# Performance work log

Measured on AMD Instinct MI355X. Metric: run time of the kernel, lower is better.

## Reference

```python
import jax, jax.numpy as jnp
import numpy as np
from jax import lax

H = 32  # hidden size (hardcoded in the torch module)

def setup_inputs() -> dict:
    key = jax.random.key(0)
    ks = jax.random.split(key, 7)
    B, T, I = 2048, 512, 64
    s = 1.0 / np.sqrt(H)  # torch nn.LSTM default init scale
    return {
        "x": jax.random.normal(ks[0], (B, T, I), dtype=jnp.float32),
        "W_ih": jax.random.uniform(ks[1], (4 * H, I), jnp.float32, -s, s),
        "W_hh": jax.random.uniform(ks[2], (4 * H, H), jnp.float32, -s, s),
        "b_ih": jax.random.uniform(ks[3], (4 * H,), jnp.float32, -s, s),
        "b_hh": jax.random.uniform(ks[4], (4 * H,), jnp.float32, -s, s),
        "W_fc": jax.random.uniform(ks[5], (1, H), jnp.float32, -s, s),
        "b_fc": jax.random.uniform(ks[6], (1,), jnp.float32, -s, s),
    }

def _lstm_last_h(x, W_ih, W_hh, b_ih, b_hh):
    B = x.shape[0]
    # Precompute input projections for all timesteps: [B, T, 4H] -> [T, B, 4H]
    xg = jnp.einsum('bti,gi->btg', x, W_ih) + (b_ih + b_hh)
    xg = jnp.transpose(xg, (1, 0, 2))

    def step(carry, xt):
        h, c = carry
        g = xt + h @ W_hh.T  # [B, 4H]
        i = jax.nn.sigmoid(g[:, 0 * H:1 * H])
        f = jax.nn.sigmoid(g[:, 1 * H:2 * H])
        gg = jnp.tanh(g[:, 2 * H:3 * H])
        o = jax.nn.sigmoid(g[:, 3 * H:4 * H])
        c = f * c + i * gg
        h = o * jnp.tanh(c)
        return (h, c), None

    init = (jnp.zeros((B, H), x.dtype), jnp.zeros((B, H), x.dtype))
    (h, _), _ = lax.scan(step, init, xg)
    return h  # [B, H], last timestep hidden state

def reference(x, W_ih, W_hh, b_ih, b_hh, W_fc, b_fc):
    # Dropout is identity in eval mode; only the last timestep feeds fc.
    h = _lstm_last_h(x, W_ih, W_hh, b_ih, b_hh)
    return h @ W_fc.T + b_fc  # [B, 1]
```

## Files before the change

kernel.cpp:

```cpp
#include <hip/hip_runtime.h>

typedef __attribute__((ext_vector_type(8))) short short8;
typedef __attribute__((ext_vector_type(4))) float f32x4;

#define LOG2E 1.44269504088896340736f

__device__ __forceinline__ unsigned short f2bf(float f) {
    union { float f; unsigned u; } a; a.f = f;
    unsigned r = a.u + 0x7fffu + ((a.u >> 16) & 1u);
    return (unsigned short)(r >> 16);
}
__device__ __forceinline__ unsigned pk2(float x, float y) {
    return (unsigned)f2bf(x) | ((unsigned)f2bf(y) << 16);
}
__device__ __forceinline__ float sigm(float x) {
    return __builtin_amdgcn_rcpf(1.0f + __builtin_amdgcn_exp2f(-LOG2E * x));
}

__global__ __launch_bounds__(256, 1) void lstm_fused(
    const float* __restrict__ x,
    const float* __restrict__ Wih,
    const float* __restrict__ Whh,
    const float* __restrict__ bih,
    const float* __restrict__ bhh,
    const float* __restrict__ Wfc,
    const float* __restrict__ bfc,
    float* __restrict__ out)
{
    __shared__ unsigned short Wlds[128 * 80];
    __shared__ float xg_sh[4 * 2 * 16 * 132];
    __shared__ alignas(64) unsigned short hbuf[4 * 64];

    const int tid  = threadIdx.x;
    const int lane = tid & 63;
    const int wv   = tid >> 6;
    const int b0   = blockIdx.x * 8 + wv * 2;
    const int m    = lane & 15;
    const int quad = lane >> 4;
    const int cc   = lane & 31;
    const int rb   = lane >> 5;

    {
        const float4* w4 = (const float4*)Wih;
        unsigned* wl = (unsigned*)Wlds;
        #pragma unroll
        for (int i = 0; i < 8; i++) {
            int fi = tid * 8 + i;
            int g  = fi >> 4;
            int k  = (fi & 15) << 2;
            float4 v = w4[fi];
            wl[g * 40 + (k >> 1) + 0] = pk2(v.x, v.y);
            wl[g * 40 + (k >> 1) + 1] = pk2(v.z, v.w);
        }
    }

    short8 Bh[8];
    #pragma unroll
    for (int t = 0; t < 8; t++) {
        const float4* wr = (const float4*)(Whh + (size_t)(16 * t + m) * 32 + quad * 8);
        float4 va = wr[0], vb = wr[1];
        union { short8 v; unsigned u[4]; } B;
        B.u[0] = pk2(va.x, va.y); B.u[1] = pk2(va.z, va.w);
        B.u[2] = pk2(vb.x, vb.y); B.u[3] = pk2(vb.z, vb.w);
        Bh[t] = B.v;
    }

    float biasv[8];
    #pragma unroll
    for (int n = 0; n < 8; n++) biasv[n] = bih[16 * n + m] + bhh[16 * n + m];

    const bool b4 = (lane & 16) != 0;

    __syncthreads();

    const float* xrow0 = x + ((size_t)b0 * 512 + m) * 64;
    const float* xrow1 = xrow0 + 512 * 64;
    float* xgw = xg_sh + wv * 4224;
    unsigned short* hw = hbuf + wv * 64;

    hw[lane] = 0;
    float c = 0.0f, h = 0.0f;
    const f32x4 z4 = {0.f, 0.f, 0.f, 0.f};

    float4 p0, p1, p2, p3, q0, q1, q2, q3;
    {
        const float4* r0 = (const float4*)xrow0;
        const float4* r1 = (const float4*)xrow1;
        p0 = r0[quad * 2];     p1 = r0[quad * 2 + 1];
        p2 = r0[8 + quad * 2]; p3 = r0[8 + quad * 2 + 1];
        q0 = r1[quad * 2];     q1 = r1[quad * 2 + 1];
        q2 = r1[8 + quad * 2]; q3 = r1[8 + quad * 2 + 1];
    }

    for (int ch = 0; ch < 32; ++ch) {
        union { short8 v; unsigned u[4]; } A0, A1, C0, C1;
        A0.u[0] = pk2(p0.x, p0.y); A0.u[1] = pk2(p0.z, p0.w);
        A0.u[2] = pk2(p1.x, p1.y); A0.u[3] = pk2(p1.z, p1.w);
        A1.u[0] = pk2(p2.x, p2.y); A1.u[1] = pk2(p2.z, p2.w);
        A1.u[2] = pk2(p3.x, p3.y); A1.u[3] = pk2(p3.z, p3.w);
        C0.u[0] = pk2(q0.x, q0.y); C0.u[1] = pk2(q0.z, q0.w);
        C0.u[2] = pk2(q1.x, q1.y); C0.u[3] = pk2(q1.z, q1.w);
        C1.u[0] = pk2(q2.x, q2.y); C1.u[1] = pk2(q2.z, q2.w);
        C1.u[2] = pk2(q3.x, q3.y); C1.u[3] = pk2(q3.z, q3.w);

        {
            const int chn = (ch < 31) ? ch + 1 : 31;
            const float4* n0 = (const float4*)(xrow0 + (size_t)chn * 1024);
            const float4* n1 = (const float4*)(xrow1 + (size_t)chn * 1024);
            p0 = n0[quad * 2];     p1 = n0[quad * 2 + 1];
            p2 = n0[8 + quad * 2]; p3 = n0[8 + quad * 2 + 1];
            q0 = n1[quad * 2];     q1 = n1[quad * 2 + 1];
            q2 = n1[8 + quad * 2]; q3 = n1[8 + quad * 2 + 1];
        }

        #pragma unroll
        for (int n = 0; n < 8; n++) {
            const short8 B0 = *(const short8*)&Wlds[(16 * n + m) * 80 + quad * 8];
            const short8 B1 = *(const short8*)&Wlds[(16 * n + m) * 80 + 32 + quad * 8];
            f32x4 ar0 = {0.f, 0.f, 0.f, 0.f};
            ar0 = __builtin_amdgcn_mfma_f32_16x16x32_bf16(A0.v, B0, ar0, 0, 0, 0);
            ar0 = __builtin_amdgcn_mfma_f32_16x16x32_bf16(A1.v, B1, ar0, 0, 0, 0);
            f32x4 ar1 = {0.f, 0.f, 0.f, 0.f};
            ar1 = __builtin_amdgcn_mfma_f32_16x16x32_bf16(C0.v, B0, ar1, 0, 0, 0);
            ar1 = __builtin_amdgcn_mfma_f32_16x16x32_bf16(C1.v, B1, ar1, 0, 0, 0);
            const int pos = ((n & 1) << 6) + 4 * m + (n >> 1);
            #pragma unroll
            for (int r = 0; r < 4; r++) {
                xgw[(quad * 4 + r) * 132 + pos]        = ar0[r] + biasv[n];
                xgw[2112 + (quad * 4 + r) * 132 + pos] = ar1[r] + biasv[n];
            }
        }

        #pragma unroll
        for (int tt = 0; tt < 16; ++tt) {
            const short8 abf = *(const short8*)&hw[((m >> 3) << 5) + quad * 8];
            const f32x4 a0 = __builtin_amdgcn_mfma_f32_16x16x32_bf16(abf, Bh[0], z4, 0, 0, 0);
            const f32x4 a1 = __builtin_amdgcn_mfma_f32_16x16x32_bf16(abf, Bh[1], z4, 0, 0, 0);
            const f32x4 a2 = __builtin_amdgcn_mfma_f32_16x16x32_bf16(abf, Bh[2], z4, 0, 0, 0);
            const f32x4 a3 = __builtin_amdgcn_mfma_f32_16x16x32_bf16(abf, Bh[3], z4, 0, 0, 0);
            const f32x4 a4 = __builtin_amdgcn_mfma_f32_16x16x32_bf16(abf, Bh[4], z4, 0, 0, 0);
            const f32x4 a5 = __builtin_amdgcn_mfma_f32_16x16x32_bf16(abf, Bh[5], z4, 0, 0, 0);
            const f32x4 a6 = __builtin_amdgcn_mfma_f32_16x16x32_bf16(abf, Bh[6], z4, 0, 0, 0);
            const f32x4 a7 = __builtin_amdgcn_mfma_f32_16x16x32_bf16(abf, Bh[7], z4, 0, 0, 0);
            const float hi = b4 ? a1[0] : a0[0];
            const float hf = b4 ? a3[0] : a2[0];
            const float hg = b4 ? a5[0] : a4[0];
            const float ho = b4 ? a7[0] : a6[0];

            const f32x4 xg4 = *(const f32x4*)&xgw[rb * 2112 + tt * 132 + 4 * cc];
            const float gi = xg4[0] + hi;
            const float gf = xg4[1] + hf;
            const float gg = xg4[2] + hg;
            const float go = xg4[3] + ho;

            const float iv = sigm(gi);
            const float fv = sigm(gf);
            const float gv = fmaf(2.0f, sigm(2.0f * gg), -1.0f);
            const float ov = sigm(go);
            c = fmaf(fv, c, iv * gv);
            const float th = fmaf(2.0f, sigm(2.0f * c), -1.0f);
            h = ov * th;
            hw[lane] = f2bf(h);
        }
    }

    float p = h * Wfc[cc];
    #pragma unroll
    for (int msk = 16; msk >= 1; msk >>= 1) p += __shfl_xor(p, msk);
    if ((lane & 31) == 0) out[b0 + rb] = p + bfc[0];
}

extern "C" void kernel_launch(void* const* d_in, const int* in_sizes, int n_in,
                              void* d_out, int out_size, void* d_ws, size_t ws_size,
                              hipStream_t stream) {
    const float* x   = (const float*)d_in[0];
    const float* Wih = (const float*)d_in[1];
    const float* Whh = (const float*)d_in[2];
    const float* bih = (const float*)d_in[3];
    const float* bhh = (const float*)d_in[4];
    const float* Wfc = (const float*)d_in[5];
    const float* bfc = (const float*)d_in[6];
    float* out = (float*)d_out;
    lstm_fused<<<dim3(256), dim3(256), 0, stream>>>(x, Wih, Whh, bih, bhh, Wfc, bfc, out);
}
```

Before: 419.7 us.

## Map one batch row per wave and run two blocks per CU

Measured after the change: 431.4 us. 1.03x slower.

```diff
diff --git a/kernel.cpp b/kernel.cpp
--- a/kernel.cpp
+++ b/kernel.cpp
@@ -17,7 +17,7 @@
     return __builtin_amdgcn_rcpf(1.0f + __builtin_amdgcn_exp2f(-LOG2E * x));
 }
 
-__global__ __launch_bounds__(256, 1) void lstm_fused(
+__global__ __launch_bounds__(256, 2) void lstm_fused(
     const float* __restrict__ x,
     const float* __restrict__ Wih,
     const float* __restrict__ Whh,
@@ -28,17 +28,16 @@
     float* __restrict__ out)
 {
     __shared__ unsigned short Wlds[128 * 80];
-    __shared__ float xg_sh[4 * 2 * 16 * 132];
+    __shared__ float xg_sh[4 * 16 * 132];
     __shared__ alignas(64) unsigned short hbuf[4 * 64];
 
     const int tid  = threadIdx.x;
     const int lane = tid & 63;
     const int wv   = tid >> 6;
-    const int b0   = blockIdx.x * 8 + wv * 2;
+    const int b0   = blockIdx.x * 4 + wv;
     const int m    = lane & 15;
     const int quad = lane >> 4;
     const int cc   = lane & 31;
-    const int rb   = lane >> 5;
 
     {
         const float4* w4 = (const float4*)Wih;
@@ -73,44 +72,33 @@
 
     __syncthreads();
 
-    const float* xrow0 = x + ((size_t)b0 * 512 + m) * 64;
-    const float* xrow1 = xrow0 + 512 * 64;
-    float* xgw = xg_sh + wv * 4224;
+    const float* xrow = x + ((size_t)b0 * 512 + m) * 64;
+    float* xgw = xg_sh + wv * 2112;
     unsigned short* hw = hbuf + wv * 64;
 
     hw[lane] = 0;
     float c = 0.0f, h = 0.0f;
     const f32x4 z4 = {0.f, 0.f, 0.f, 0.f};
 
-    float4 p0, p1, p2, p3, q0, q1, q2, q3;
+    float4 p0, p1, p2, p3;
     {
-        const float4* r0 = (const float4*)xrow0;
-        const float4* r1 = (const float4*)xrow1;
+        const float4* r0 = (const float4*)xrow;
         p0 = r0[quad * 2];     p1 = r0[quad * 2 + 1];
         p2 = r0[8 + quad * 2]; p3 = r0[8 + quad * 2 + 1];
-        q0 = r1[quad * 2];     q1 = r1[quad * 2 + 1];
-        q2 = r1[8 + quad * 2]; q3 = r1[8 + quad * 2 + 1];
     }
 
     for (int ch = 0; ch < 32; ++ch) {
-        union { short8 v; unsigned u[4]; } A0, A1, C0, C1;
+        union { short8 v; unsigned u[4]; } A0, A1;
         A0.u[0] = pk2(p0.x, p0.y); A0.u[1] = pk2(p0.z, p0.w);
         A0.u[2] = pk2(p1.x, p1.y); A0.u[3] = pk2(p1.z, p1.w);
         A1.u[0] = pk2(p2.x, p2.y); A1.u[1] = pk2(p2.z, p2.w);
         A1.u[2] = pk2(p3.x, p3.y); A1.u[3] = pk2(p3.z, p3.w);
-        C0.u[0] = pk2(q0.x, q0.y); C0.u[1] = pk2(q0.z, q0.w);
-        C0.u[2] = pk2(q1.x, q1.y); C0.u[3] = pk2(q1.z, q1.w);
-        C1.u[0] = pk2(q2.x, q2.y); C1.u[1] = pk2(q2.z, q2.w);
-        C1.u[2] = pk2(q3.x, q3.y); C1.u[3] = pk2(q3.z, q3.w);
 
         {
             const int chn = (ch < 31) ? ch + 1 : 31;
-            const float4* n0 = (const float4*)(xrow0 + (size_t)chn * 1024);
-            const float4* n1 = (const float4*)(xrow1 + (size_t)chn * 1024);
+            const float4* n0 = (const float4*)(xrow + (size_t)chn * 1024);
             p0 = n0[quad * 2];     p1 = n0[quad * 2 + 1];
             p2 = n0[8 + quad * 2]; p3 = n0[8 + quad * 2 + 1];
-            q0 = n1[quad * 2];     q1 = n1[quad * 2 + 1];
-            q2 = n1[8 + quad * 2]; q3 = n1[8 + quad * 2 + 1];
         }
 
         #pragma unroll
@@ -120,20 +108,16 @@
             f32x4 ar0 = {0.f, 0.f, 0.f, 0.f};
             ar0 = __builtin_amdgcn_mfma_f32_16x16x32_bf16(A0.v, B0, ar0, 0, 0, 0);
             ar0 = __builtin_amdgcn_mfma_f32_16x16x32_bf16(A1.v, B1, ar0, 0, 0, 0);
-            f32x4 ar1 = {0.f, 0.f, 0.f, 0.f};
-            ar1 = __builtin_amdgcn_mfma_f32_16x16x32_bf16(C0.v, B0, ar1, 0, 0, 0);
-            ar1 = __builtin_amdgcn_mfma_f32_16x16x32_bf16(C1.v, B1, ar1, 0, 0, 0);
             const int pos = ((n & 1) << 6) + 4 * m + (n >> 1);
             #pragma unroll
             for (int r = 0; r < 4; r++) {
-                xgw[(quad * 4 + r) * 132 + pos]        = ar0[r] + biasv[n];
-                xgw[2112 + (quad * 4 + r) * 132 + pos] = ar1[r] + biasv[n];
+                xgw[(quad * 4 + r) * 132 + pos] = ar0[r] + biasv[n];
             }
         }
 
         #pragma unroll
         for (int tt = 0; tt < 16; ++tt) {
-            const short8 abf = *(const short8*)&hw[((m >> 3) << 5) + quad * 8];
+            const short8 abf = *(const short8*)&hw[quad * 8];
             const f32x4 a0 = __builtin_amdgcn_mfma_f32_16x16x32_bf16(abf, Bh[0], z4, 0, 0, 0);
             const f32x4 a1 = __builtin_amdgcn_mfma_f32_16x16x32_bf16(abf, Bh[1], z4, 0, 0, 0);
             const f32x4 a2 = __builtin_amdgcn_mfma_f32_16x16x32_bf16(abf, Bh[2], z4, 0, 0, 0);
@@ -147,7 +131,7 @@
             const float hg = b4 ? a5[0] : a4[0];
             const float ho = b4 ? a7[0] : a6[0];
 
-            const f32x4 xg4 = *(const f32x4*)&xgw[rb * 2112 + tt * 132 + 4 * cc];
+            const f32x4 xg4 = *(const f32x4*)&xgw[tt * 132 + 4 * cc];
             const float gi = xg4[0] + hi;
             const float gf = xg4[1] + hf;
             const float gg = xg4[2] + hg;
@@ -167,7 +151,7 @@
     float p = h * Wfc[cc];
     #pragma unroll
     for (int msk = 16; msk >= 1; msk >>= 1) p += __shfl_xor(p, msk);
-    if ((lane & 31) == 0) out[b0 + rb] = p + bfc[0];
+    if (lane == 0) out[b0] = p + bfc[0];
 }
 
 extern "C" void kernel_launch(void* const* d_in, const int* in_sizes, int n_in,
@@ -181,5 +165,5 @@
     const float* Wfc = (const float*)d_in[5];
     const float* bfc = (const float*)d_in[6];
     float* out = (float*)d_out;
-    lstm_fused<<<dim3(256), dim3(256), 0, stream>>>(x, Wih, Whh, bih, bhh, Wfc, bfc, out);
+    lstm_fused<<<dim3(512), dim3(256), 0, stream>>>(x, Wih, Whh, bih, bhh, Wfc, bfc, out);
 }
```

## Keep LSTM hidden state in registers via transposed MFMA and lane shuffles

Applied to the files above, without the earlier changes.

Result: slower. 504.8 us (+20.3%).

```diff
diff --git a/kernel.cpp b/kernel.cpp
--- a/kernel.cpp
+++ b/kernel.cpp
@@ -5,13 +5,10 @@
 
 #define LOG2E 1.44269504088896340736f
 
-__device__ __forceinline__ unsigned short f2bf(float f) {
-    union { float f; unsigned u; } a; a.f = f;
-    unsigned r = a.u + 0x7fffu + ((a.u >> 16) & 1u);
-    return (unsigned short)(r >> 16);
-}
-__device__ __forceinline__ unsigned pk2(float x, float y) {
-    return (unsigned)f2bf(x) | ((unsigned)f2bf(y) << 16);
+__device__ __forceinline__ unsigned pkcvt(float lo, float hi) {
+    unsigned r;
+    asm("v_cvt_pk_bf16_f32 %0, %1, %2" : "=v"(r) : "v"(lo), "v"(hi));
+    return r;
 }
 __device__ __forceinline__ float sigm(float x) {
     return __builtin_amdgcn_rcpf(1.0f + __builtin_amdgcn_exp2f(-LOG2E * x));
@@ -28,17 +25,16 @@
     float* __restrict__ out)
 {
     __shared__ unsigned short Wlds[128 * 80];
-    __shared__ float xg_sh[4 * 2 * 16 * 132];
-    __shared__ alignas(64) unsigned short hbuf[4 * 64];
+    __shared__ float xg_sh[4 * 4768];
 
     const int tid  = threadIdx.x;
     const int lane = tid & 63;
     const int wv   = tid >> 6;
     const int b0   = blockIdx.x * 8 + wv * 2;
     const int m    = lane & 15;
-    const int quad = lane >> 4;
-    const int cc   = lane & 31;
-    const int rb   = lane >> 5;
+    const int q    = lane >> 4;
+    const int g    = m & 3;
+    const int rm   = (m >> 3) & 1;
 
     {
         const float4* w4 = (const float4*)Wih;
@@ -46,128 +42,161 @@
         #pragma unroll
         for (int i = 0; i < 8; i++) {
             int fi = tid * 8 + i;
-            int g  = fi >> 4;
+            int gg = fi >> 4;
             int k  = (fi & 15) << 2;
             float4 v = w4[fi];
-            wl[g * 40 + (k >> 1) + 0] = pk2(v.x, v.y);
-            wl[g * 40 + (k >> 1) + 1] = pk2(v.z, v.w);
-        }
-    }
-
-    short8 Bh[8];
+            wl[gg * 40 + (k >> 1) + 0] = pkcvt(v.x, v.y);
+            wl[gg * 40 + (k >> 1) + 1] = pkcvt(v.z, v.w);
+        }
+    }
+
+    short8 Wr[8];
     #pragma unroll
     for (int t = 0; t < 8; t++) {
-        const float4* wr = (const float4*)(Whh + (size_t)(16 * t + m) * 32 + quad * 8);
+        const int gr = (t >> 1) * 32 + 8 * (m >> 2) + (t & 1) * 4 + (m & 3);
+        const float4* wr = (const float4*)(Whh + (size_t)gr * 32 + q * 8);
         float4 va = wr[0], vb = wr[1];
         union { short8 v; unsigned u[4]; } B;
-        B.u[0] = pk2(va.x, va.y); B.u[1] = pk2(va.z, va.w);
-        B.u[2] = pk2(vb.x, vb.y); B.u[3] = pk2(vb.z, vb.w);
-        Bh[t] = B.v;
+        B.u[0] = pkcvt(va.x, va.y); B.u[1] = pkcvt(va.z, va.w);
+        B.u[2] = pkcvt(vb.x, vb.y); B.u[3] = pkcvt(vb.z, vb.w);
+        Wr[t] = B.v;
     }
 
     float biasv[8];
     #pragma unroll
     for (int n = 0; n < 8; n++) biasv[n] = bih[16 * n + m] + bhh[16 * n + m];
 
-    const bool b4 = (lane & 16) != 0;
-
     __syncthreads();
 
     const float* xrow0 = x + ((size_t)b0 * 512 + m) * 64;
     const float* xrow1 = xrow0 + 512 * 64;
-    float* xgw = xg_sh + wv * 4224;
-    unsigned short* hw = hbuf + wv * 64;
-
-    hw[lane] = 0;
-    float c = 0.0f, h = 0.0f;
+    float* xgw = xg_sh + wv * 4768;
+
+    float c0 = 0.0f, c1 = 0.0f, h0 = 0.0f, h1 = 0.0f;
     const f32x4 z4 = {0.f, 0.f, 0.f, 0.f};
 
     float4 p0, p1, p2, p3, q0, q1, q2, q3;
     {
         const float4* r0 = (const float4*)xrow0;
         const float4* r1 = (const float4*)xrow1;
-        p0 = r0[quad * 2];     p1 = r0[quad * 2 + 1];
-        p2 = r0[8 + quad * 2]; p3 = r0[8 + quad * 2 + 1];
-        q0 = r1[quad * 2];     q1 = r1[quad * 2 + 1];
-        q2 = r1[8 + quad * 2]; q3 = r1[8 + quad * 2 + 1];
-    }
+        p0 = r0[q * 2];     p1 = r0[q * 2 + 1];
+        p2 = r0[8 + q * 2]; p3 = r0[8 + q * 2 + 1];
+        q0 = r1[q * 2];     q1 = r1[q * 2 + 1];
+        q2 = r1[8 + q * 2]; q3 = r1[8 + q * 2 + 1];
+    }
+
+    const float* xb = xgw + rm * 2384 + q * 36 + g * 8;
+    const bool tsel = (g & 2) != 0;
+    const bool jsel = (g & 1) != 0;
 
     for (int ch = 0; ch < 32; ++ch) {
         union { short8 v; unsigned u[4]; } A0, A1, C0, C1;
-        A0.u[0] = pk2(p0.x, p0.y); A0.u[1] = pk2(p0.z, p0.w);
-        A0.u[2] = pk2(p1.x, p1.y); A0.u[3] = pk2(p1.z, p1.w);
-        A1.u[0] = pk2(p2.x, p2.y); A1.u[1] = pk2(p2.z, p2.w);
-        A1.u[2] = pk2(p3.x, p3.y); A1.u[3] = pk2(p3.z, p3.w);
-        C0.u[0] = pk2(q0.x, q0.y); C0.u[1] = pk2(q0.z, q0.w);
-        C0.u[2] = pk2(q1.x, q1.y); C0.u[3] = pk2(q1.z, q1.w);
-        C1.u[0] = pk2(q2.x, q2.y); C1.u[1] = pk2(q2.z, q2.w);
-        C1.u[2] = pk2(q3.x, q3.y); C1.u[3] = pk2(q3.z, q3.w);
+        A0.u[0] = pkcvt(p0.x, p0.y); A0.u[1] = pkcvt(p0.z, p0.w);
+        A0.u[2] = pkcvt(p1.x, p1.y); A0.u[3] = pkcvt(p1.z, p1.w);
+        A1.u[0] = pkcvt(p2.x, p2.y); A1.u[1] = pkcvt(p2.z, p2.w);
+        A1.u[2] = pkcvt(p3.x, p3.y); A1.u[3] = pkcvt(p3.z, p3.w);
+        C0.u[0] = pkcvt(q0.x, q0.y); C0.u[1] = pkcvt(q0.z, q0.w);
+        C0.u[2] = pkcvt(q1.x, q1.y); C0.u[3] = pkcvt(q1.z, q1.w);
+        C1.u[0] = pkcvt(q2.x, q2.y); C1.u[1] = pkcvt(q2.z, q2.w);
+        C1.u[2] = pkcvt(q3.x, q3.y); C1.u[3] = pkcvt(q3.z, q3.w);
 
         {
             const int chn = (ch < 31) ? ch + 1 : 31;
             const float4* n0 = (const float4*)(xrow0 + (size_t)chn * 1024);
             const float4* n1 = (const float4*)(xrow1 + (size_t)chn * 1024);
-            p0 = n0[quad * 2];     p1 = n0[quad * 2 + 1];
-            p2 = n0[8 + quad * 2]; p3 = n0[8 + quad * 2 + 1];
-            q0 = n1[quad * 2];     q1 = n1[quad * 2 + 1];
-            q2 = n1[8 + quad * 2]; q3 = n1[8 + quad * 2 + 1];
+            p0 = n0[q * 2];     p1 = n0[q * 2 + 1];
+            p2 = n0[8 + q * 2]; p3 = n0[8 + q * 2 + 1];
+            q0 = n1[q * 2];     q1 = n1[q * 2 + 1];
+            q2 = n1[8 + q * 2]; q3 = n1[8 + q * 2 + 1];
         }
 
         #pragma unroll
         for (int n = 0; n < 8; n++) {
-            const short8 B0 = *(const short8*)&Wlds[(16 * n + m) * 80 + quad * 8];
-            const short8 B1 = *(const short8*)&Wlds[(16 * n + m) * 80 + 32 + quad * 8];
-            f32x4 ar0 = {0.f, 0.f, 0.f, 0.f};
+            const short8 B0 = *(const short8*)&Wlds[(16 * n + m) * 80 + q * 8];
+            const short8 B1 = *(const short8*)&Wlds[(16 * n + m) * 80 + 32 + q * 8];
+            f32x4 ar0 = z4, ar1 = z4;
             ar0 = __builtin_amdgcn_mfma_f32_16x16x32_bf16(A0.v, B0, ar0, 0, 0, 0);
             ar0 = __builtin_amdgcn_mfma_f32_16x16x32_bf16(A1.v, B1, ar0, 0, 0, 0);
-            f32x4 ar1 = {0.f, 0.f, 0.f, 0.f};
             ar1 = __builtin_amdgcn_mfma_f32_16x16x32_bf16(C0.v, B0, ar1, 0, 0, 0);
             ar1 = __builtin_amdgcn_mfma_f32_16x16x32_bf16(C1.v, B1, ar1, 0, 0, 0);
-            const int pos = ((n & 1) << 6) + 4 * m + (n >> 1);
+            const int so = ((n & 1) * 2 + (m >> 3)) * 36 + (m & 7) * 4 + (n >> 1);
             #pragma unroll
             for (int r = 0; r < 4; r++) {
-                xgw[(quad * 4 + r) * 132 + pos]        = ar0[r] + biasv[n];
-                xgw[2112 + (quad * 4 + r) * 132 + pos] = ar1[r] + biasv[n];
+                xgw[(4 * q + r) * 148 + so]        = ar0[r] + biasv[n];
+                xgw[2384 + (4 * q + r) * 148 + so] = ar1[r] + biasv[n];
             }
         }
 
         #pragma unroll
         for (int tt = 0; tt < 16; ++tt) {
-            const short8 abf = *(const short8*)&hw[((m >> 3) << 5) + quad * 8];
-            const f32x4 a0 = __builtin_amdgcn_mfma_f32_16x16x32_bf16(abf, Bh[0], z4, 0, 0, 0);
-            const f32x4 a1 = __builtin_amdgcn_mfma_f32_16x16x32_bf16(abf, Bh[1], z4, 0, 0, 0);
-            const f32x4 a2 = __builtin_amdgcn_mfma_f32_16x16x32_bf16(abf, Bh[2], z4, 0, 0, 0);
-            const f32x4 a3 = __builtin_amdgcn_mfma_f32_16x16x32_bf16(abf, Bh[3], z4, 0, 0, 0);
-            const f32x4 a4 = __builtin_amdgcn_mfma_f32_16x16x32_bf16(abf, Bh[4], z4, 0, 0, 0);
-            const f32x4 a5 = __builtin_amdgcn_mfma_f32_16x16x32_bf16(abf, Bh[5], z4, 0, 0, 0);
-            const f32x4 a6 = __builtin_amdgcn_mfma_f32_16x16x32_bf16(abf, Bh[6], z4, 0, 0, 0);
-            const f32x4 a7 = __builtin_amdgcn_mfma_f32_16x16x32_bf16(abf, Bh[7], z4, 0, 0, 0);
-            const float hi = b4 ? a1[0] : a0[0];
-            const float hf = b4 ? a3[0] : a2[0];
-            const float hg = b4 ? a5[0] : a4[0];
-            const float ho = b4 ? a7[0] : a6[0];
-
-            const f32x4 xg4 = *(const f32x4*)&xgw[rb * 2112 + tt * 132 + 4 * cc];
-            const float gi = xg4[0] + hi;
-            const float gf = xg4[1] + hf;
-            const float gg = xg4[2] + hg;
-            const float go = xg4[3] + ho;
-
-            const float iv = sigm(gi);
-            const float fv = sigm(gf);
-            const float gv = fmaf(2.0f, sigm(2.0f * gg), -1.0f);
-            const float ov = sigm(go);
-            c = fmaf(fv, c, iv * gv);
-            const float th = fmaf(2.0f, sigm(2.0f * c), -1.0f);
-            h = ov * th;
-            hw[lane] = f2bf(h);
-        }
-    }
-
-    float p = h * Wfc[cc];
-    #pragma unroll
-    for (int msk = 16; msk >= 1; msk >>= 1) p += __shfl_xor(p, msk);
-    if ((lane & 31) == 0) out[b0 + rb] = p + bfc[0];
+            const int own = (int)pkcvt(h0, h1);
+            const int x1  = __shfl_xor(own, 1);
+            const int plo = jsel ? x1 : own;
+            const int phi = jsel ? own : x1;
+            const int qlo = __shfl_xor(plo, 2);
+            const int qhi = __shfl_xor(phi, 2);
+            union { short8 v; int u[4]; } H;
+            H.u[0] = tsel ? qlo : plo;
+            H.u[1] = tsel ? qhi : phi;
+            H.u[2] = tsel ? plo : qlo;
+            H.u[3] = tsel ? phi : qhi;
+
+            const f32x4 a0 = __builtin_amdgcn_mfma_f32_16x16x32_bf16(Wr[0], H.v, z4, 0, 0, 0);
+            const f32x4 a1 = __builtin_amdgcn_mfma_f32_16x16x32_bf16(Wr[1], H.v, z4, 0, 0, 0);
+            const f32x4 a2 = __builtin_amdgcn_mfma_f32_16x16x32_bf16(Wr[2], H.v, z4, 0, 0, 0);
+            const f32x4 a3 = __builtin_amdgcn_mfma_f32_16x16x32_bf16(Wr[3], H.v, z4, 0, 0, 0);
+            const f32x4 a4 = __builtin_amdgcn_mfma_f32_16x16x32_bf16(Wr[4], H.v, z4, 0, 0, 0);
+            const f32x4 a5 = __builtin_amdgcn_mfma_f32_16x16x32_bf16(Wr[5], H.v, z4, 0, 0, 0);
+            const f32x4 a6 = __builtin_amdgcn_mfma_f32_16x16x32_bf16(Wr[6], H.v, z4, 0, 0, 0);
+            const f32x4 a7 = __builtin_amdgcn_mfma_f32_16x16x32_bf16(Wr[7], H.v, z4, 0, 0, 0);
+
+            const f32x4 xgA = *(const f32x4*)(xb + tt * 148);
+            const f32x4 xgB = *(const f32x4*)(xb + tt * 148 + 4);
+
+            float vi0, vi1, vf0, vf1, vg0, vg1, vo0, vo1;
+            {
+                const float e0 = tsel ? a1[0] : a0[0], e1 = tsel ? a1[1] : a0[1];
+                const float e2 = tsel ? a1[2] : a0[2], e3 = tsel ? a1[3] : a0[3];
+                vi0 = jsel ? e2 : e0; vi1 = jsel ? e3 : e1;
+            }
+            {
+                const float e0 = tsel ? a3[0] : a2[0], e1 = tsel ? a3[1] : a2[1];
+                const float e2 = tsel ? a3[2] : a2[2], e3 = tsel ? a3[3] : a2[3];
+                vf0 = jsel ? e2 : e0; vf1 = jsel ? e3 : e1;
+            }
+            {
+                const float e0 = tsel ? a5[0] : a4[0], e1 = tsel ? a5[1] : a4[1];
+                const float e2 = tsel ? a5[2] : a4[2], e3 = tsel ? a5[3] : a4[3];
+                vg0 = jsel ? e2 : e0; vg1 = jsel ? e3 : e1;
+            }
+            {
+                const float e0 = tsel ? a7[0] : a6[0], e1 = tsel ? a7[1] : a6[1];
+                const float e2 = tsel ? a7[2] : a6[2], e3 = tsel ? a7[3] : a6[3];
+                vo0 = jsel ? e2 : e0; vo1 = jsel ? e3 : e1;
+            }
+
+            const float gi0 = xgA[0] + vi0, gf0 = xgA[1] + vf0;
+            const float gg0 = xgA[2] + vg0, go0 = xgA[3] + vo0;
+            const float iv0 = sigm(gi0), fv0 = sigm(gf0), ov0 = sigm(go0);
+            const float gv0 = fmaf(2.0f, sigm(2.0f * gg0), -1.0f);
+            c0 = fmaf(fv0, c0, iv0 * gv0);
+            h0 = ov0 * fmaf(2.0f, sigm(2.0f * c0), -1.0f);
+            const float gi1 = xgB[0] + vi1, gf1 = xgB[1] + vf1;
+            const float gg1 = xgB[2] + vg1, go1 = xgB[3] + vo1;
+            const float iv1 = sigm(gi1), fv1 = sigm(gf1), ov1 = sigm(go1);
+            const float gv1 = fmaf(2.0f, sigm(2.0f * gg1), -1.0f);
+            c1 = fmaf(fv1, c1, iv1 * gv1);
+            h1 = ov1 * fmaf(2.0f, sigm(2.0f * c1), -1.0f);
+        }
+    }
+
+    float p = h0 * Wfc[8 * q + 2 * g] + h1 * Wfc[8 * q + 2 * g + 1];
+    p += __shfl_xor(p, 1);
+    p += __shfl_xor(p, 2);
+    p += __shfl_xor(p, 16);
+    p += __shfl_xor(p, 32);
+    if (lane == 0)      out[b0]     = p + bfc[0];
+    else if (lane == 8) out[b0 + 1] = p + bfc[0];
 }
 
 extern "C" void kernel_launch(void* const* d_in, const int* in_sizes, int n_in,
```
